# Optimization experiments

Measured on AMD Instinct MI355X. Metric: run time of the kernel, lower is better.

## Reference

```python
import jax, jax.numpy as jnp
import numpy as np

D_MODEL = 1024
NUM_HEADS = 16
D_K = D_MODEL // NUM_HEADS
NEG = jnp.float32(-1e9)  # finite stand-in for -inf to keep softmax NaN-free on fully masked rows


def setup_inputs() -> dict:
    key = jax.random.key(0)
    ks = jax.random.split(key, 7)
    B, N_q, N_kv = 2, 2048, 2048
    x = jax.random.normal(ks[0], (B, N_q, D_MODEL), dtype=jnp.float32)
    K = jax.random.normal(ks[1], (B, NUM_HEADS, N_kv, D_K), dtype=jnp.float32)
    V = jax.random.normal(ks[2], (B, NUM_HEADS, N_kv, D_K), dtype=jnp.float32)
    # pad masks: True = keep. Ensure first kv position is always valid.
    kv_pad_mask = jax.random.uniform(ks[3], (B, 1, 1, N_kv)) > 0.1
    kv_pad_mask = kv_pad_mask.at[..., 0].set(True)
    q_pad_mask = jax.random.uniform(ks[4], (B, 1, N_q, 1)) > 0.1
    # params (torch Linear, bias=False); stored as [in, out] so y = x @ W
    Wq = jax.random.normal(ks[5], (D_MODEL, D_MODEL), dtype=jnp.float32) / np.sqrt(D_MODEL)
    Wo = jax.random.normal(ks[6], (D_MODEL, D_MODEL), dtype=jnp.float32) / np.sqrt(D_MODEL)
    return {"x": x, "K": K, "V": V, "Wq": Wq, "Wo": Wo,
            "kv_pad_mask": kv_pad_mask, "q_pad_mask": q_pad_mask}


def reference(x, K, V, Wq, Wo, kv_pad_mask, q_pad_mask):
    B, N_q, D = x.shape
    H, d_k = NUM_HEADS, D_K
    # Q projection and split into heads: [B, H, N_q, d_k]
    Q = (x @ Wq).reshape(B, N_q, H, d_k).transpose(0, 2, 1, 3)
    scores = jnp.einsum('bhqd,bhkd->bhqk', Q, K) / np.sqrt(d_k).astype(np.float32)
    keep = q_pad_mask & kv_pad_mask  # broadcast to [B,1,N_q,N_kv]
    scores = jnp.where(keep, scores, NEG)
    probs = jax.nn.softmax(scores, axis=-1)
    attn = jnp.einsum('bhqk,bhkd->bhqd', probs, V)  # [B,H,N_q,d_k]
    attn = attn.transpose(0, 2, 1, 3).reshape(B, N_q, H * d_k)
    return attn @ Wo
```

## Files before the change

### kernel.cpp

```cpp
#include <hip/hip_runtime.h>
#include <hip/hip_bf16.h>
#include <stdint.h>

typedef __hip_bfloat16 bf16;
typedef __attribute__((ext_vector_type(8))) short short8;
typedef __attribute__((ext_vector_type(4))) short s16x4;
typedef __attribute__((ext_vector_type(4))) float floatx4;

#define MFMA16(a, b, c) __builtin_amdgcn_mfma_f32_16x16x32_bf16(a, b, c, 0, 0, 0)
#define WAIT_VM6 3958
#define WAIT_VM4 3956
#define WAIT_VM0 3952

__device__ __forceinline__ void async_lds16(const void* g, void* l) {
  __builtin_amdgcn_global_load_lds((__attribute__((address_space(1))) const void*)g,
                                   (__attribute__((address_space(3))) void*)l, 16, 0, 0);
}

__device__ __forceinline__ unsigned rne2(float a, float b) {
  unsigned ua = __float_as_uint(a), ub = __float_as_uint(b);
  ua = ua + 0x7FFFu + ((ua >> 16) & 1u);
  ub = ub + 0x7FFFu + ((ub >> 16) & 1u);
  return (ua >> 16) | (ub & 0xFFFF0000u);
}

__global__ __launch_bounds__(256) void prep_k(const float* __restrict__ x, bf16* __restrict__ xb,
                                              const float* __restrict__ Kf, bf16* __restrict__ Kb,
                                              const float* __restrict__ Wq, bf16* __restrict__ WqT,
                                              const float* __restrict__ Wo, bf16* __restrict__ WoT,
                                              const float* __restrict__ V, bf16* __restrict__ VTb,
                                              const int* __restrict__ kvm, const int* __restrict__ qm,
                                              float* __restrict__ kvB, float* __restrict__ qB) {
  __shared__ float tile[64][65];
  int bid = blockIdx.x, tid = threadIdx.x;
  if (bid < 8192) {
    const float* s; bf16* d; int g = bid;
    if (g < 4096) { s = x; d = xb; } else { s = Kf; d = Kb; g -= 4096; }
    int i = (g * 256 + tid) * 4;
    float4 v = *(const float4*)(s + i);
    uint2 o = {rne2(v.x, v.y), rne2(v.z, v.w)};
    *(uint2*)(d + i) = o;
    return;
  }
  if (bid < 9744 - 16) {
    const float* s; bf16* d; int r0, c0, R, C;
    if (bid < 8704) {
      int idx = bid - 8192;
      s = (idx >> 8) ? Wo : Wq; d = (idx >> 8) ? WoT : WqT;
      int rem = idx & 255;
      r0 = (rem & 15) * 64; c0 = (rem >> 4) * 64; R = 1024; C = 1024;
    } else {
      int idx = bid - 8704;
      int m = idx >> 5;
      s = V + (size_t)m * 2048 * 64; d = VTb + (size_t)m * 2048 * 64;
      r0 = (idx & 31) * 64; c0 = 0; R = 2048; C = 64;
    }
    int tr = tid >> 2, tg = tid & 3;
#pragma unroll
    for (int k = 0; k < 4; ++k) {
      int col = tg * 16 + k * 4;
      float4 v = *(const float4*)(s + (size_t)(r0 + tr) * C + c0 + col);
      tile[tr][col] = v.x; tile[tr][col + 1] = v.y;
      tile[tr][col + 2] = v.z; tile[tr][col + 3] = v.w;
    }
    __syncthreads();
    int orow = tid >> 2, ch = tid & 3;
    bf16* drow = d + (size_t)(c0 + orow) * R + r0;
    uint4 w0, w1;
    w0.x = rne2(tile[ch * 8 + 0][orow], tile[ch * 8 + 1][orow]);
    w0.y = rne2(tile[ch * 8 + 2][orow], tile[ch * 8 + 3][orow]);
    w0.z = rne2(tile[ch * 8 + 4][orow], tile[ch * 8 + 5][orow]);
    w0.w = rne2(tile[ch * 8 + 6][orow], tile[ch * 8 + 7][orow]);
    w1.x = rne2(tile[32 + ch * 8 + 0][orow], tile[32 + ch * 8 + 1][orow]);
    w1.y = rne2(tile[32 + ch * 8 + 2][orow], tile[32 + ch * 8 + 3][orow]);
    w1.z = rne2(tile[32 + ch * 8 + 4][orow], tile[32 + ch * 8 + 5][orow]);
    w1.w = rne2(tile[32 + ch * 8 + 6][orow], tile[32 + ch * 8 + 7][orow]);
    *(uint4*)(drow + ch * 8) = w0;
    *(uint4*)(drow + 32 + ch * 8) = w1;
    return;
  }
  int i = (bid - (9744 - 16)) * 256 + tid;
  kvB[i] = kvm[i] ? 0.0f : -3000.0f;
  qB[i]  = qm[i]  ? 0.0f : -3000.0f;
}

__device__ __forceinline__ void storeC(bf16* C, size_t i, float v) { C[i] = __float2bfloat16(v); }
__device__ __forceinline__ void storeC(float* C, size_t i, float v) { C[i] = v; }

template <typename OT>
__global__ __launch_bounds__(256) void gemm_bt_k(const bf16* __restrict__ A,
                                                 const bf16* __restrict__ BT,
                                                 OT* __restrict__ C,
                                                 int M, int N, int K, float scale) {
  __shared__ __align__(16) bf16 As[2][128 * 64];
  __shared__ __align__(16) bf16 Bs[2][64 * 64];
  int tid = threadIdx.x;
  int wave = tid >> 6, lane = tid & 63;
  int quad = lane >> 4, lm = lane & 15;
  int wm = wave >> 1, wn = wave & 1;
  int row0 = blockIdx.y * 128, col0 = blockIdx.x * 64;

  floatx4 acc[4][2];
#pragma unroll
  for (int mt = 0; mt < 4; ++mt)
#pragma unroll
    for (int nt = 0; nt < 2; ++nt) acc[mt][nt] = (floatx4){0.f, 0.f, 0.f, 0.f};

  auto stage = [&](int buf, int k0) {
#pragma unroll
    for (int ch = 0; ch < 4; ++ch) {
      int e = (wave * 4 + ch) * 512 + lane * 8;
      int r = e >> 6, c16 = (e & 63) >> 3;
      int sc = (c16 ^ (r & 7)) * 8;
      async_lds16(A + (size_t)(row0 + r) * K + k0 + sc, &As[buf][(wave * 4 + ch) * 512]);
    }
#pragma unroll
    for (int ch = 0; ch < 2; ++ch) {
      int e = (wave * 2 + ch) * 512 + lane * 8;
      int r = e >> 6, c16 = (e & 63) >> 3;
      int sc = (c16 ^ (r & 7)) * 8;
      async_lds16(BT + (size_t)(col0 + r) * K + k0 + sc, &Bs[buf][(wave * 2 + ch) * 512]);
    }
  };

  int niter = K >> 6;
  stage(0, 0);
  for (int i = 0; i < niter; ++i) {
    __builtin_amdgcn_s_barrier();
    if (i + 1 < niter) {
      stage((i + 1) & 1, (i + 1) << 6);
      __builtin_amdgcn_s_waitcnt(WAIT_VM6);
    } else {
      __builtin_amdgcn_s_waitcnt(WAIT_VM0);
    }
    __builtin_amdgcn_s_barrier();
    const bf16* Ac = As[i & 1];
    const bf16* Bc = Bs[i & 1];
    int sw = lm & 7;
#pragma unroll
    for (int ks = 0; ks < 64; ks += 32) {
      short8 af[4], bfr[2];
#pragma unroll
      for (int mt = 0; mt < 4; ++mt) {
        int R = wm * 64 + mt * 16 + lm;
        af[mt] = *(const short8*)&Ac[R * 64 + ((((ks >> 3) + quad) ^ sw) * 8)];
      }
#pragma unroll
      for (int nt = 0; nt < 2; ++nt) {
        int R = wn * 32 + nt * 16 + lm;
        bfr[nt] = *(const short8*)&Bc[R * 64 + ((((ks >> 3) + quad) ^ sw) * 8)];
      }
#pragma unroll
      for (int mt = 0; mt < 4; ++mt)
#pragma unroll
        for (int nt = 0; nt < 2; ++nt)
          acc[mt][nt] = MFMA16(af[mt], bfr[nt], acc[mt][nt]);
    }
  }
#pragma unroll
  for (int mt = 0; mt < 4; ++mt)
#pragma unroll
    for (int nt = 0; nt < 2; ++nt)
#pragma unroll
      for (int j = 0; j < 4; ++j) {
        int rr = row0 + wm * 64 + mt * 16 + quad * 4 + j;
        int cc = col0 + wn * 32 + nt * 16 + lm;
        storeC(C, (size_t)rr * N + cc, acc[mt][nt][j] * scale);
      }
}

__global__ __launch_bounds__(256, 4) void attn_k(const bf16* __restrict__ Q,
                                                 const bf16* __restrict__ Km,
                                                 const bf16* __restrict__ VT,
                                                 const float* __restrict__ qB,
                                                 const float* __restrict__ kvB,
                                                 bf16* __restrict__ Opart,
                                                 float* __restrict__ lpart) {
  const float TINY = 9.313225746154785e-10f;
  __shared__ __align__(16) bf16 Ks[2][64 * 64];
  __shared__ __align__(16) bf16 Vs[2][64 * 64];
  __shared__ __align__(16) float kvBs[1024];

  int tid = threadIdx.x;
  int wave = tid >> 6, lane = tid & 63;
  int quad = lane >> 4, lm = lane & 15;
  int qb = blockIdx.x & 15, slice = blockIdx.x >> 4;
  int h = blockIdx.y, b = blockIdx.z;
  int q0 = qb * 128 + wave * 32;
  int kvbeg = slice * 1024;

  const bf16* kbase = Km + (size_t)(b * 16 + h) * 2048 * 64;
  const bf16* vbase = VT + (size_t)(b * 16 + h) * 64 * 2048;
  const float* kvBb = kvB + b * 2048;

  {
    float4 v0 = *(const float4*)(kvBb + kvbeg + tid * 4);
    *(float4*)&kvBs[tid * 4] = v0;
  }

  short8 aq[2][2];
  float qbias[2];
#pragma unroll
  for (int g = 0; g < 2; ++g) {
    const bf16* qp = Q + (size_t)(b * 2048 + q0 + g * 16 + lm) * 1024 + h * 64 + quad * 8;
    aq[g][0] = *(const short8*)qp;
    aq[g][1] = *(const short8*)(qp + 32);
    qbias[g] = qB[b * 2048 + q0 + g * 16 + lm];
  }

  short8 ones;
#pragma unroll
  for (int i = 0; i < 8; ++i) ones[i] = (short)0x3F80;

  floatx4 o_acc[2][4];
  floatx4 l_acc[2];
#pragma unroll
  for (int g = 0; g < 2; ++g) {
    l_acc[g] = (floatx4){0.f, 0.f, 0.f, 0.f};
#pragma unroll
    for (int t = 0; t < 4; ++t) o_acc[g][t] = (floatx4){0.f, 0.f, 0.f, 0.f};
  }

  union S8U { short8 s8; s16x4 h[2]; unsigned u[4]; };

  auto stageKV = [&](int buf, int kv0) {
#pragma unroll
    for (int c = 0; c < 2; ++c) {
      int o = (wave * 2 + c) * 1024 + lane * 16;
      int r = o >> 7;
      int g16 = (o >> 4) & 7;
      int sc = ((g16 ^ (r & 7)) * 8);
      async_lds16(kbase + (size_t)(kv0 + r) * 64 + sc, &Ks[buf][(wave * 2 + c) * 512]);
      async_lds16(vbase + (size_t)r * 2048 + kv0 + sc, &Vs[buf][(wave * 2 + c) * 512]);
    }
  };

  auto compute = [&](int buf, int rel) {
    const bf16* Kc = Ks[buf];
    const bf16* Vc = Vs[buf];
    S8U pf[2][2];
#pragma unroll
    for (int t = 0; t < 4; ++t) {
      int R = t * 16 + lm, sw = lm & 7;
      short8 kf0 = *(const short8*)&Kc[R * 64 + ((quad ^ sw) * 8)];
      short8 kf1 = *(const short8*)&Kc[R * 64 + (((quad + 4) ^ sw) * 8)];
      floatx4 zb = *(const floatx4*)&kvBs[rel + t * 16 + quad * 4];
#pragma unroll
      for (int g = 0; g < 2; ++g) {
        floatx4 z;
#pragma unroll
        for (int j = 0; j < 4; ++j) z[j] = zb[j] + qbias[g];
        z = MFMA16(kf0, aq[g][0], z);
        z = MFMA16(kf1, aq[g][1], z);
        float p0 = __builtin_amdgcn_exp2f(z[0]) + TINY;
        float p1 = __builtin_amdgcn_exp2f(z[1]) + TINY;
        float p2 = __builtin_amdgcn_exp2f(z[2]) + TINY;
        float p3 = __builtin_amdgcn_exp2f(z[3]) + TINY;
        pf[g][t >> 1].u[(t & 1) * 2 + 0] = rne2(p0, p1);
        pf[g][t >> 1].u[(t & 1) * 2 + 1] = rne2(p2, p3);
      }
    }
#pragma unroll
    for (int t = 0; t < 4; ++t) {
      int D = t * 16 + lm, sw = lm & 7;
      int hoff = (quad & 1) * 4, qh = quad >> 1;
      S8U vf0, vf1;
      vf0.h[0] = *(const s16x4*)&Vc[D * 64 + (((0 + qh) ^ sw) * 8) + hoff];
      vf0.h[1] = *(const s16x4*)&Vc[D * 64 + (((2 + qh) ^ sw) * 8) + hoff];
      vf1.h[0] = *(const s16x4*)&Vc[D * 64 + (((4 + qh) ^ sw) * 8) + hoff];
      vf1.h[1] = *(const s16x4*)&Vc[D * 64 + (((6 + qh) ^ sw) * 8) + hoff];
#pragma unroll
      for (int g = 0; g < 2; ++g) {
        o_acc[g][t] = MFMA16(vf0.s8, pf[g][0].s8, o_acc[g][t]);
        o_acc[g][t] = MFMA16(vf1.s8, pf[g][1].s8, o_acc[g][t]);
      }
    }
#pragma unroll
    for (int g = 0; g < 2; ++g) {
      l_acc[g] = MFMA16(ones, pf[g][0].s8, l_acc[g]);
      l_acc[g] = MFMA16(ones, pf[g][1].s8, l_acc[g]);
    }
  };

  __syncthreads();
  stageKV(0, kvbeg);
  for (int i = 0; i < 16; i += 2) {
    __builtin_amdgcn_s_barrier();
    stageKV(1, kvbeg + (i + 1) * 64);
    __builtin_amdgcn_s_waitcnt(WAIT_VM4);
    __builtin_amdgcn_s_barrier();
    compute(0, i * 64);

    __builtin_amdgcn_s_barrier();
    if (i + 2 < 16) {
      stageKV(0, kvbeg + (i + 2) * 64);
      __builtin_amdgcn_s_waitcnt(WAIT_VM4);
    } else {
      __builtin_amdgcn_s_waitcnt(WAIT_VM0);
    }
    __builtin_amdgcn_s_barrier();
    compute(1, (i + 1) * 64);
  }
  bf16* Op = Opart + (size_t)slice * 4194304u;
#pragma unroll
  for (int g = 0; g < 2; ++g) {
    int q = b * 2048 + q0 + g * 16 + lm;
    bf16* orow = Op + (size_t)q * 1024 + h * 64;
#pragma unroll
    for (int t = 0; t < 4; ++t) {
      uint2 ov = {rne2(o_acc[g][t][0], o_acc[g][t][1]),
                  rne2(o_acc[g][t][2], o_acc[g][t][3])};
      *(uint2*)(orow + t * 16 + quad * 4) = ov;
    }
    if (quad == 0)
      lpart[((size_t)slice * 4096 + (size_t)q) * 16 + h] = l_acc[g][0];
  }
}

__global__ void combine_k(const bf16* __restrict__ Opart, const float* __restrict__ lpart,
                          bf16* __restrict__ out) {
  int i = (blockIdx.x * 256 + threadIdx.x) * 8;
  int bq = i >> 10, h = (i >> 6) & 15;
  float l = lpart[bq * 16 + h] + lpart[65536 + bq * 16 + h];
  float rl = 1.0f / l;
  float acc[8];
#pragma unroll
  for (int e = 0; e < 8; ++e) acc[e] = 0.f;
#pragma unroll
  for (int s = 0; s < 2; ++s) {
    uint4 u = *(const uint4*)(Opart + s * 4194304 + i);
    acc[0] += __uint_as_float(u.x << 16); acc[1] += __uint_as_float(u.x & 0xFFFF0000u);
    acc[2] += __uint_as_float(u.y << 16); acc[3] += __uint_as_float(u.y & 0xFFFF0000u);
    acc[4] += __uint_as_float(u.z << 16); acc[5] += __uint_as_float(u.z & 0xFFFF0000u);
    acc[6] += __uint_as_float(u.w << 16); acc[7] += __uint_as_float(u.w & 0xFFFF0000u);
  }
  uint4 o = {rne2(acc[0] * rl, acc[1] * rl), rne2(acc[2] * rl, acc[3] * rl),
             rne2(acc[4] * rl, acc[5] * rl), rne2(acc[6] * rl, acc[7] * rl)};
  *(uint4*)(out + i) = o;
}

extern "C" void kernel_launch(void* const* d_in, const int* in_sizes, int n_in,
                              void* d_out, int out_size, void* d_ws, size_t ws_size,
                              hipStream_t stream) {
  const float* x  = (const float*)d_in[0];
  const float* K  = (const float*)d_in[1];
  const float* V  = (const float*)d_in[2];
  const float* Wq = (const float*)d_in[3];
  const float* Wo = (const float*)d_in[4];
  const int* kvm  = (const int*)d_in[5];
  const int* qm   = (const int*)d_in[6];

  char* w = (char*)d_ws;
  bf16* xb    = (bf16*)(w);
  bf16* attnb = xb;
  bf16* Qb    = (bf16*)(w + (8u << 20));
  bf16* Kb    = (bf16*)(w + (16u << 20));
  bf16* VTb   = (bf16*)(w + (24u << 20));
  bf16* WqT   = (bf16*)(w + (32u << 20));
  bf16* WoT   = (bf16*)(w + (34u << 20));
  float* qB   = (float*)(w + (36u << 20));
  float* kvB  = (float*)(w + (36u << 20) + 16384);
  bf16* Opart = (bf16*)(w + (40u << 20));
  float* lpart = (float*)(w + (72u << 20));

  const float SCL2 = 0.18033688011112042f;

  prep_k<<<9744, 256, 0, stream>>>(x, xb, K, Kb, Wq, WqT, Wo, WoT, V, VTb, kvm, qm, kvB, qB);
  gemm_bt_k<bf16><<<dim3(16, 32), 256, 0, stream>>>(xb, WqT, Qb, 4096, 1024, 1024, SCL2);
  attn_k<<<dim3(32, 16, 2), 256, 0, stream>>>(Qb, Kb, VTb, qB, kvB, Opart, lpart);
  combine_k<<<2048, 256, 0, stream>>>(Opart, lpart, attnb);
  gemm_bt_k<float><<<dim3(16, 32), 256, 0, stream>>>(attnb, WoT, (float*)d_out, 4096, 1024, 1024, 1.0f);
}
```

Baseline: 206.8 us.

## Triple-buffer GEMM loads, fold q-mask into exp scale, use hardware bf16 pack

The GEMM kernel moves from double to triple buffering, keeping two async K-tiles in flight with an adjusted vmcnt wait, to hide global-load latency better. In attention, the query pad bias added to every score is replaced by a 0/1 multiplier fused into an fma after exp2, which removes per-element adds. Manual round-to-nearest bf16 packing is swapped for the hardware cvt_pk_bf16_f32 builtin where it exists. The extra GEMM buffer raises LDS use to 72KB per block, which may lower occupancy. Masked query rows now give uniform TINY weights instead of a bias-shifted softmax, which changes numerics slightly.

Result: faster. 201.1 us (-2.7%).

```diff
diff --git a/kernel.cpp b/kernel.cpp
--- a/kernel.cpp
+++ b/kernel.cpp
@@ -8,9 +8,10 @@
 typedef __attribute__((ext_vector_type(4))) float floatx4;
 
 #define MFMA16(a, b, c) __builtin_amdgcn_mfma_f32_16x16x32_bf16(a, b, c, 0, 0, 0)
-#define WAIT_VM6 3958
-#define WAIT_VM4 3956
-#define WAIT_VM0 3952
+#define WAIT_VM12 3964
+#define WAIT_VM6  3958
+#define WAIT_VM4  3956
+#define WAIT_VM0  3952
 
 __device__ __forceinline__ void async_lds16(const void* g, void* l) {
   __builtin_amdgcn_global_load_lds((__attribute__((address_space(1))) const void*)g,
@@ -22,6 +23,15 @@
   ua = ua + 0x7FFFu + ((ua >> 16) & 1u);
   ub = ub + 0x7FFFu + ((ub >> 16) & 1u);
   return (ua >> 16) | (ub & 0xFFFF0000u);
+}
+
+__device__ __forceinline__ unsigned pk2(float a, float b) {
+#if __has_builtin(__builtin_amdgcn_cvt_pk_bf16_f32)
+  auto r = __builtin_amdgcn_cvt_pk_bf16_f32(a, b);
+  return __builtin_bit_cast(unsigned, r);
+#else
+  return rne2(a, b);
+#endif
 }
 
 __global__ __launch_bounds__(256) void prep_k(const float* __restrict__ x, bf16* __restrict__ xb,
@@ -30,7 +40,7 @@
                                               const float* __restrict__ Wo, bf16* __restrict__ WoT,
                                               const float* __restrict__ V, bf16* __restrict__ VTb,
                                               const int* __restrict__ kvm, const int* __restrict__ qm,
-                                              float* __restrict__ kvB, float* __restrict__ qB) {
+                                              float* __restrict__ kvB, float* __restrict__ qS) {
   __shared__ float tile[64][65];
   int bid = blockIdx.x, tid = threadIdx.x;
   if (bid < 8192) {
@@ -81,7 +91,7 @@
   }
   int i = (bid - (9744 - 16)) * 256 + tid;
   kvB[i] = kvm[i] ? 0.0f : -3000.0f;
-  qB[i]  = qm[i]  ? 0.0f : -3000.0f;
+  qS[i]  = qm[i]  ? 1.0f : 0.0f;
 }
 
 __device__ __forceinline__ void storeC(bf16* C, size_t i, float v) { C[i] = __float2bfloat16(v); }
@@ -92,8 +102,8 @@
                                                  const bf16* __restrict__ BT,
                                                  OT* __restrict__ C,
                                                  int M, int N, int K, float scale) {
-  __shared__ __align__(16) bf16 As[2][128 * 64];
-  __shared__ __align__(16) bf16 Bs[2][64 * 64];
+  __shared__ __align__(16) bf16 As[3 * 128 * 64];
+  __shared__ __align__(16) bf16 Bs[3 * 64 * 64];
   int tid = threadIdx.x;
   int wave = tid >> 6, lane = tid & 63;
   int quad = lane >> 4, lm = lane & 15;
@@ -106,36 +116,43 @@
 #pragma unroll
     for (int nt = 0; nt < 2; ++nt) acc[mt][nt] = (floatx4){0.f, 0.f, 0.f, 0.f};
 
-  auto stage = [&](int buf, int k0) {
+  auto stage = [&](int buf, int it) {
+    int k0 = it << 6;
 #pragma unroll
     for (int ch = 0; ch < 4; ++ch) {
       int e = (wave * 4 + ch) * 512 + lane * 8;
       int r = e >> 6, c16 = (e & 63) >> 3;
       int sc = (c16 ^ (r & 7)) * 8;
-      async_lds16(A + (size_t)(row0 + r) * K + k0 + sc, &As[buf][(wave * 4 + ch) * 512]);
+      async_lds16(A + (size_t)(row0 + r) * K + k0 + sc, &As[buf * 8192 + (wave * 4 + ch) * 512]);
     }
 #pragma unroll
     for (int ch = 0; ch < 2; ++ch) {
       int e = (wave * 2 + ch) * 512 + lane * 8;
       int r = e >> 6, c16 = (e & 63) >> 3;
       int sc = (c16 ^ (r & 7)) * 8;
-      async_lds16(BT + (size_t)(col0 + r) * K + k0 + sc, &Bs[buf][(wave * 2 + ch) * 512]);
+      async_lds16(BT + (size_t)(col0 + r) * K + k0 + sc, &Bs[buf * 4096 + (wave * 2 + ch) * 512]);
     }
   };
 
   int niter = K >> 6;
   stage(0, 0);
+  stage(1, 1);
+  int put = 2, get = 0;
   for (int i = 0; i < niter; ++i) {
     __builtin_amdgcn_s_barrier();
-    if (i + 1 < niter) {
-      stage((i + 1) & 1, (i + 1) << 6);
+    if (i + 2 < niter) {
+      stage(put, i + 2);
+      put = (put == 2) ? 0 : put + 1;
+      __builtin_amdgcn_s_waitcnt(WAIT_VM12);
+    } else if (i + 1 < niter) {
       __builtin_amdgcn_s_waitcnt(WAIT_VM6);
     } else {
       __builtin_amdgcn_s_waitcnt(WAIT_VM0);
     }
     __builtin_amdgcn_s_barrier();
-    const bf16* Ac = As[i & 1];
-    const bf16* Bc = Bs[i & 1];
+    const bf16* Ac = As + get * 8192;
+    const bf16* Bc = Bs + get * 4096;
+    get = (get == 2) ? 0 : get + 1;
     int sw = lm & 7;
 #pragma unroll
     for (int ks = 0; ks < 64; ks += 32) {
@@ -172,13 +189,13 @@
 __global__ __launch_bounds__(256, 4) void attn_k(const bf16* __restrict__ Q,
                                                  const bf16* __restrict__ Km,
                                                  const bf16* __restrict__ VT,
-                                                 const float* __restrict__ qB,
+                                                 const float* __restrict__ qS,
                                                  const float* __restrict__ kvB,
                                                  bf16* __restrict__ Opart,
                                                  float* __restrict__ lpart) {
   const float TINY = 9.313225746154785e-10f;
-  __shared__ __align__(16) bf16 Ks[2][64 * 64];
-  __shared__ __align__(16) bf16 Vs[2][64 * 64];
+  __shared__ __align__(16) bf16 Ks[2 * 64 * 64];
+  __shared__ __align__(16) bf16 Vs[2 * 64 * 64];
   __shared__ __align__(16) float kvBs[1024];
 
   int tid = threadIdx.x;
@@ -199,13 +216,13 @@
   }
 
   short8 aq[2][2];
-  float qbias[2];
+  float qscl[2];
 #pragma unroll
   for (int g = 0; g < 2; ++g) {
     const bf16* qp = Q + (size_t)(b * 2048 + q0 + g * 16 + lm) * 1024 + h * 64 + quad * 8;
     aq[g][0] = *(const short8*)qp;
     aq[g][1] = *(const short8*)(qp + 32);
-    qbias[g] = qB[b * 2048 + q0 + g * 16 + lm];
+    qscl[g] = qS[b * 2048 + q0 + g * 16 + lm];
   }
 
   short8 ones;
@@ -230,14 +247,14 @@
       int r = o >> 7;
       int g16 = (o >> 4) & 7;
       int sc = ((g16 ^ (r & 7)) * 8);
-      async_lds16(kbase + (size_t)(kv0 + r) * 64 + sc, &Ks[buf][(wave * 2 + c) * 512]);
-      async_lds16(vbase + (size_t)r * 2048 + kv0 + sc, &Vs[buf][(wave * 2 + c) * 512]);
+      async_lds16(kbase + (size_t)(kv0 + r) * 64 + sc, &Ks[buf * 4096 + (wave * 2 + c) * 512]);
+      async_lds16(vbase + (size_t)r * 2048 + kv0 + sc, &Vs[buf * 4096 + (wave * 2 + c) * 512]);
     }
   };
 
   auto compute = [&](int buf, int rel) {
-    const bf16* Kc = Ks[buf];
-    const bf16* Vc = Vs[buf];
+    const bf16* Kc = Ks + buf * 4096;
+    const bf16* Vc = Vs + buf * 4096;
     S8U pf[2][2];
 #pragma unroll
     for (int t = 0; t < 4; ++t) {
@@ -247,17 +264,15 @@
       floatx4 zb = *(const floatx4*)&kvBs[rel + t * 16 + quad * 4];
 #pragma unroll
       for (int g = 0; g < 2; ++g) {
-        floatx4 z;
-#pragma unroll
-        for (int j = 0; j < 4; ++j) z[j] = zb[j] + qbias[g];
+        floatx4 z = zb;
         z = MFMA16(kf0, aq[g][0], z);
         z = MFMA16(kf1, aq[g][1], z);
-        float p0 = __builtin_amdgcn_exp2f(z[0]) + TINY;
-        float p1 = __builtin_amdgcn_exp2f(z[1]) + TINY;
-        float p2 = __builtin_amdgcn_exp2f(z[2]) + TINY;
-        float p3 = __builtin_amdgcn_exp2f(z[3]) + TINY;
-        pf[g][t >> 1].u[(t & 1) * 2 + 0] = rne2(p0, p1);
-        pf[g][t >> 1].u[(t & 1) * 2 + 1] = rne2(p2, p3);
+        float p0 = fmaf(__builtin_amdgcn_exp2f(z[0]), qscl[g], TINY);
+        float p1 = fmaf(__builtin_amdgcn_exp2f(z[1]), qscl[g], TINY);
+        float p2 = fmaf(__builtin_amdgcn_exp2f(z[2]), qscl[g], TINY);
+        float p3 = fmaf(__builtin_amdgcn_exp2f(z[3]), qscl[g], TINY);
+        pf[g][t >> 1].u[(t & 1) * 2 + 0] = pk2(p0, p1);
+        pf[g][t >> 1].u[(t & 1) * 2 + 1] = pk2(p2, p3);
       }
     }
 #pragma unroll
@@ -308,8 +323,8 @@
     bf16* orow = Op + (size_t)q * 1024 + h * 64;
 #pragma unroll
     for (int t = 0; t < 4; ++t) {
-      uint2 ov = {rne2(o_acc[g][t][0], o_acc[g][t][1]),
-                  rne2(o_acc[g][t][2], o_acc[g][t][3])};
+      uint2 ov = {pk2(o_acc[g][t][0], o_acc[g][t][1]),
+                  pk2(o_acc[g][t][2], o_acc[g][t][3])};
       *(uint2*)(orow + t * 16 + quad * 4) = ov;
     }
     if (quad == 0)
@@ -358,16 +373,16 @@
   bf16* VTb   = (bf16*)(w + (24u << 20));
   bf16* WqT   = (bf16*)(w + (32u << 20));
   bf16* WoT   = (bf16*)(w + (34u << 20));
-  float* qB   = (float*)(w + (36u << 20));
+  float* qS   = (float*)(w + (36u << 20));
   float* kvB  = (float*)(w + (36u << 20) + 16384);
   bf16* Opart = (bf16*)(w + (40u << 20));
   float* lpart = (float*)(w + (72u << 20));
 
   const float SCL2 = 0.18033688011112042f;
 
-  prep_k<<<9744, 256, 0, stream>>>(x, xb, K, Kb, Wq, WqT, Wo, WoT, V, VTb, kvm, qm, kvB, qB);
+  prep_k<<<9744, 256, 0, stream>>>(x, xb, K, Kb, Wq, WqT, Wo, WoT, V, VTb, kvm, qm, kvB, qS);
   gemm_bt_k<bf16><<<dim3(16, 32), 256, 0, stream>>>(xb, WqT, Qb, 4096, 1024, 1024, SCL2);
-  attn_k<<<dim3(32, 16, 2), 256, 0, stream>>>(Qb, Kb, VTb, qB, kvB, Opart, lpart);
+  attn_k<<<dim3(32, 16, 2), 256, 0, stream>>>(Qb, Kb, VTb, qS, kvB, Opart, lpart);
   combine_k<<<2048, 256, 0, stream>>>(Opart, lpart, attnb);
   gemm_bt_k<float><<<dim3(16, 32), 256, 0, stream>>>(attnb, WoT, (float*)d_out, 4096, 1024, 1024, 1.0f);
 }
```
